# Performance work log

Hardware: AMD Instinct MI355X
Metric: run time of the kernel (lower is better)

The kernel has to match this reference:

```python
import jax, jax.numpy as jnp
import numpy as np

B, N, D, H, O = 4096, 128, 64, 256, 128  # batch, memory_size, memory_dim, controller_dim, output_size


def setup_inputs() -> dict:
    key = jax.random.key(0)
    ks = jax.random.split(key, 20)
    s = 0.05
    inp = {
        "x": jax.random.normal(ks[0], (B, O), jnp.float32),
        "memory": jax.random.normal(ks[1], (B, N, D), jnp.float32),
        "h": jax.random.normal(ks[2], (B, H), jnp.float32),
        "c": jax.random.normal(ks[3], (B, H), jnp.float32),
        # LSTMCell params (torch layout: gates ordered i, f, g, o; input = x||read_vec of width O+D)
        "W_ih": jax.random.normal(ks[4], (4 * H, O + D), jnp.float32) * s,
        "W_hh": jax.random.normal(ks[5], (4 * H, H), jnp.float32) * s,
        "b_ih": jax.random.normal(ks[6], (4 * H,), jnp.float32) * s,
        "b_hh": jax.random.normal(ks[7], (4 * H,), jnp.float32) * s,
        "W_read": jax.random.normal(ks[8], (N, H), jnp.float32) * s,
        "b_read": jax.random.normal(ks[9], (N,), jnp.float32) * s,
        "W_write": jax.random.normal(ks[10], (N, H), jnp.float32) * s,
        "b_write": jax.random.normal(ks[11], (N,), jnp.float32) * s,
        "W_erase": jax.random.normal(ks[12], (D, H), jnp.float32) * s,
        "b_erase": jax.random.normal(ks[13], (D,), jnp.float32) * s,
        "W_add": jax.random.normal(ks[14], (D, H), jnp.float32) * s,
        "b_add": jax.random.normal(ks[15], (D,), jnp.float32) * s,
        "W_out": jax.random.normal(ks[16], (O, H + D), jnp.float32) * s,
        "b_out": jax.random.normal(ks[17], (O,), jnp.float32) * s,
    }
    return inp


def reference(x, memory, h, c, W_ih, W_hh, b_ih, b_hh, W_read, b_read,
              W_write, b_write, W_erase, b_erase, W_add, b_add, W_out, b_out):
    # read: softmax attention over memory rows, addressed by previous hidden state
    read_w = jax.nn.softmax(h @ W_read.T + b_read, axis=-1)          # [B, N]
    read_vec = jnp.einsum("bn,bnd->bd", read_w, memory)               # [B, D]

    # LSTMCell step (torch gate order: i, f, g, o)
    ctrl_in = jnp.concatenate([x, read_vec], axis=-1)                 # [B, O+D]
    gates = ctrl_in @ W_ih.T + b_ih + h @ W_hh.T + b_hh               # [B, 4H]
    i, f, g, o = jnp.split(gates, 4, axis=-1)
    i, f, o = jax.nn.sigmoid(i), jax.nn.sigmoid(f), jax.nn.sigmoid(o)
    g = jnp.tanh(g)
    c_new = f * c + i * g
    h_new = o * jnp.tanh(c_new)

    # write: outer-product erase/add update
    write_w = jax.nn.softmax(h_new @ W_write.T + b_write, axis=-1)    # [B, N]
    erase = jax.nn.sigmoid(h_new @ W_erase.T + b_erase)               # [B, D]
    add = jnp.tanh(h_new @ W_add.T + b_add)                           # [B, D]
    ww = write_w[:, :, None]                                          # [B, N, 1]
    mem_new = memory * (1.0 - ww * erase[:, None, :]) + ww * add[:, None, :]

    out = jnp.concatenate([h_new, read_vec], axis=-1) @ W_out.T + b_out  # [B, O]
    return (out, mem_new, h_new, c_new)
```

## Files before the change

kernel.cpp:

```cpp
#include <hip/hip_runtime.h>
#include <math.h>


typedef __attribute__((ext_vector_type(8))) short bf16x8;
typedef __attribute__((ext_vector_type(4))) float f32x4;
typedef __attribute__((ext_vector_type(4))) unsigned short us4;

#define MFMA16(a, b, c) __builtin_amdgcn_mfma_f32_16x16x32_bf16(a, b, c, 0, 0, 0)
#define GLL16(gp, lp) __builtin_amdgcn_global_load_lds( \
    (const __attribute__((address_space(1))) void*)(gp), \
    (__attribute__((address_space(3))) void*)(lp), 16, 0, 0)
#define SW(row, s) ((s) ^ ((row) & 3))

__device__ __forceinline__ float sigf(float v) { return 1.f / (1.f + __expf(-v)); }

__device__ __forceinline__ unsigned short f2bf(float f) {
    unsigned u = __builtin_bit_cast(unsigned, f);
    u = (u + 0x7FFFu + ((u >> 16) & 1u)) >> 16;
    return (unsigned short)u;
}

__global__ __launch_bounds__(256) void kA_prep(
    const float* __restrict__ Wih, const float* __restrict__ Whh,
    const float* __restrict__ bih, const float* __restrict__ bhh,
    const float* __restrict__ Wr, const float* __restrict__ br,
    const float* __restrict__ Ww, const float* __restrict__ We,
    const float* __restrict__ Wa, const float* __restrict__ bw,
    const float* __restrict__ be, const float* __restrict__ ba,
    const float* __restrict__ Wo, const float* __restrict__ x,
    const float* __restrict__ h, const float* __restrict__ mem,
    unsigned short* __restrict__ Wg, float* __restrict__ bsum,
    unsigned short* __restrict__ Wh_b, float* __restrict__ bh_b,
    unsigned short* __restrict__ Wo_b, unsigned short* __restrict__ Ag,
    unsigned short* __restrict__ Aout)
{
    __shared__ unsigned short As[16 * 32];
    __shared__ unsigned short Bs[128 * 32];
    __shared__ float sc[16][128];
    __shared__ float wL[16][128];
    __shared__ float part[16][68];

    int t = threadIdx.x;
    int wid = t >> 6, lane = t & 63;
    int cl = lane & 15, ks = lane >> 4;
    int b0 = blockIdx.x * 16;

    int idx = blockIdx.x * 256 + t;
    int stride = gridDim.x * 256;
    for (int i = idx; i < 1024 * 448; i += stride) {
        int r = i / 448, cc = i - r * 448;
        float v = (cc < 192) ? Wih[(size_t)r * 192 + cc] : Whh[(size_t)r * 256 + (cc - 192)];
        Wg[i] = f2bf(v);
    }
    for (int i = idx; i < 1024; i += stride) bsum[i] = bih[i] + bhh[i];
    for (int i = idx; i < 256 * 256; i += stride) {
        int r = i >> 8, cc = i & 255;
        float v = (r < 128) ? Ww[(size_t)r * 256 + cc]
                : (r < 192) ? We[(size_t)(r - 128) * 256 + cc]
                            : Wa[(size_t)(r - 192) * 256 + cc];
        Wh_b[i] = f2bf(v);
    }
    for (int i = idx; i < 256; i += stride)
        bh_b[i] = (i < 128) ? bw[i] : (i < 192 ? be[i - 128] : ba[i - 192]);
    for (int i = idx; i < 128 * 320; i += stride) Wo_b[i] = f2bf(Wo[i]);
    for (int i = idx; i < 4096 * 96; i += stride) {
        int row = i / 96, j = i - row * 96;
        float4 v = (j < 32) ? ((const float4*)(x + (size_t)row * 128))[j]
                            : ((const float4*)(h + (size_t)row * 256))[j - 32];
        us4 o = { f2bf(v.x), f2bf(v.y), f2bf(v.z), f2bf(v.w) };
        int col = (j < 32) ? j * 4 : 192 + (j - 32) * 4;
        *(us4*)(Ag + (size_t)row * 448 + col) = o;
    }

    int aOff = cl * 32 + SW(cl, ks) * 8;
    int bOff[4];
#pragma unroll
    for (int f = 0; f < 4; ++f) {
        int br_ = (wid * 4 + f) * 16 + cl;
        bOff[f] = br_ * 32 + SW(br_, ks) * 8;
    }
    f32x4 acc[4] = {};
    for (int kc = 0; kc < 8; ++kc) {
        __syncthreads();
        {
            int row = t >> 4, k0 = (t & 15) * 2;
            float2 hv = *(const float2*)(h + (size_t)(b0 + row) * 256 + kc * 32 + k0);
            unsigned pk = (unsigned)f2bf(hv.x) | ((unsigned)f2bf(hv.y) << 16);
            *(unsigned*)(As + row * 32 + SW(row, k0 >> 3) * 8 + (k0 & 7)) = pk;
        }
        {
            int row = t >> 1, k0 = (t & 1) * 16;
            const float4* wp = (const float4*)(Wr + (size_t)row * 256 + kc * 32 + k0);
            float4 w0 = wp[0], w1 = wp[1], w2 = wp[2], w3 = wp[3];
            us4 p0 = { f2bf(w0.x), f2bf(w0.y), f2bf(w0.z), f2bf(w0.w) };
            us4 p1 = { f2bf(w1.x), f2bf(w1.y), f2bf(w1.z), f2bf(w1.w) };
            us4 p2 = { f2bf(w2.x), f2bf(w2.y), f2bf(w2.z), f2bf(w2.w) };
            us4 p3 = { f2bf(w3.x), f2bf(w3.y), f2bf(w3.z), f2bf(w3.w) };
            int g0 = k0 >> 3;
            unsigned short* basep = Bs + row * 32;
            *(us4*)(basep + SW(row, g0) * 8)     = p0;
            *(us4*)(basep + SW(row, g0) * 8 + 4) = p1;
            *(us4*)(basep + SW(row, g0 + 1) * 8)     = p2;
            *(us4*)(basep + SW(row, g0 + 1) * 8 + 4) = p3;
        }
        __syncthreads();
        if (wid < 2) {
            bf16x8 a = *(const bf16x8*)(As + aOff);
#pragma unroll
            for (int f = 0; f < 4; ++f)
                acc[f] = MFMA16(a, *(const bf16x8*)(Bs + bOff[f]), acc[f]);
        }
    }
    if (wid < 2) {
#pragma unroll
        for (int f = 0; f < 4; ++f)
#pragma unroll
            for (int r = 0; r < 4; ++r)
                sc[ks * 4 + r][(wid * 4 + f) * 16 + cl] = acc[f][r];
    }
    __syncthreads();
    {
        int row = t >> 4, l = t & 15;
        float v[8];
#pragma unroll
        for (int j = 0; j < 8; ++j) v[j] = sc[row][l + 16 * j] + br[l + 16 * j];
        float m = v[0];
#pragma unroll
        for (int j = 1; j < 8; ++j) m = fmaxf(m, v[j]);
#pragma unroll
        for (int mk = 8; mk >= 1; mk >>= 1) m = fmaxf(m, __shfl_xor(m, mk));
        float s = 0.f;
#pragma unroll
        for (int j = 0; j < 8; ++j) { v[j] = __expf(v[j] - m); s += v[j]; }
#pragma unroll
        for (int mk = 8; mk >= 1; mk >>= 1) s += __shfl_xor(s, mk);
        float inv = 1.f / s;
#pragma unroll
        for (int j = 0; j < 8; ++j) wL[row][l + 16 * j] = v[j] * inv;
    }
    __syncthreads();

    int np = t >> 4, d4 = t & 15;
    for (int r = 0; r < 16; ++r) {
        int row = b0 + r;
        const f32x4* m4 = (const f32x4*)(mem + (size_t)row * 8192);
        f32x4 a4 = { 0.f, 0.f, 0.f, 0.f };
#pragma unroll
        for (int j = 0; j < 8; ++j) {
            float w = wL[r][np + 16 * j];
            f32x4 mv = m4[t + 256 * j];
            a4 += w * mv;
        }
        part[np][d4 * 4 + 0] = a4[0]; part[np][d4 * 4 + 1] = a4[1];
        part[np][d4 * 4 + 2] = a4[2]; part[np][d4 * 4 + 3] = a4[3];
        __syncthreads();
        if (t < 64) {
            float s = 0.f;
#pragma unroll
            for (int q = 0; q < 16; ++q) s += part[q][t];
            unsigned short bv = f2bf(s);
            Ag[(size_t)row * 448 + 128 + t] = bv;
            Aout[(size_t)row * 320 + 256 + t] = bv;
        }
        __syncthreads();
    }
}

__global__ __launch_bounds__(256) void kB_gates(
    const unsigned short* __restrict__ Ag, const unsigned short* __restrict__ Wg,
    const float* __restrict__ bsum, const float* __restrict__ c,
    float* __restrict__ h_new, float* __restrict__ c_new,
    unsigned short* __restrict__ Aout)
{
    __shared__ unsigned short As[64 * 32];
    __shared__ unsigned short Bs[256 * 32];
    int t = threadIdx.x;
    int wid = t >> 6, lane = t & 63;
    int cl = lane & 15, ks = lane >> 4;
    int b0 = blockIdx.x * 64;
    int u0 = blockIdx.y * 64;

    int arow = t >> 2;
    const unsigned short* aSrc = Ag + (size_t)(b0 + arow) * 448 + SW(arow, t & 3) * 8;
    unsigned short* aDst = As + wid * 512;
    const unsigned short* bSrc[4];
    unsigned short* bDst[4];
#pragma unroll
    for (int j = 0; j < 4; ++j) {
        int rl = (j * 256 + t) >> 2;
        int g = rl >> 6, u = rl & 63;
        bSrc[j] = Wg + (size_t)(g * 256 + u0 + u) * 448 + SW(rl, t & 3) * 8;
        bDst[j] = Bs + (j * 256 + wid * 64) * 8;
    }

    int aOff[4];
#pragma unroll
    for (int rf = 0; rf < 4; ++rf) {
        int mr = rf * 16 + cl;
        aOff[rf] = mr * 32 + SW(mr, ks) * 8;
    }
    int bOff[4];
#pragma unroll
    for (int g = 0; g < 4; ++g) {
        int br_ = g * 64 + wid * 16 + cl;
        bOff[g] = br_ * 32 + SW(br_, ks) * 8;
    }

    f32x4 acc[4][4] = {};
    for (int kc = 0; kc < 14; ++kc) {
        __syncthreads();
        GLL16(aSrc, aDst);
        GLL16(bSrc[0], bDst[0]); GLL16(bSrc[1], bDst[1]);
        GLL16(bSrc[2], bDst[2]); GLL16(bSrc[3], bDst[3]);
        aSrc += 32;
#pragma unroll
        for (int j = 0; j < 4; ++j) bSrc[j] += 32;
        __syncthreads();
        bf16x8 a[4], b[4];
#pragma unroll
        for (int rf = 0; rf < 4; ++rf) a[rf] = *(const bf16x8*)(As + aOff[rf]);
#pragma unroll
        for (int g = 0; g < 4; ++g) b[g] = *(const bf16x8*)(Bs + bOff[g]);
#pragma unroll
        for (int rf = 0; rf < 4; ++rf)
#pragma unroll
            for (int g = 0; g < 4; ++g)
                acc[rf][g] = MFMA16(a[rf], b[g], acc[rf][g]);
    }

    int unit = u0 + wid * 16 + cl;
    float bi = bsum[unit], bf_ = bsum[256 + unit];
    float bg = bsum[512 + unit], bo_ = bsum[768 + unit];
#pragma unroll
    for (int rf = 0; rf < 4; ++rf) {
#pragma unroll
        for (int r = 0; r < 4; ++r) {
            int row = b0 + rf * 16 + ks * 4 + r;
            float iv = sigf(acc[rf][0][r] + bi);
            float fv = sigf(acc[rf][1][r] + bf_);
            float gv = tanhf(acc[rf][2][r] + bg);
            float ov = sigf(acc[rf][3][r] + bo_);
            float cv = fv * c[(size_t)row * 256 + unit] + iv * gv;
            float hv = ov * tanhf(cv);
            c_new[(size_t)row * 256 + unit] = cv;
            h_new[(size_t)row * 256 + unit] = hv;
            Aout[(size_t)row * 320 + unit] = f2bf(hv);
        }
    }
}

__global__ __launch_bounds__(256) void kC_heads_out_mem(
    const unsigned short* __restrict__ Aout, const unsigned short* __restrict__ Wh_b,
    const unsigned short* __restrict__ Wo_b, const float* __restrict__ bh_b,
    const float* __restrict__ bo, const float* __restrict__ mem,
    float* __restrict__ outp, float* __restrict__ mem_new)
{
    __shared__ unsigned short As[16 * 32];
    __shared__ unsigned short Bh[256 * 32];
    __shared__ unsigned short Bo[128 * 32];
    __shared__ float sc[16][256];
    __shared__ __align__(16) float wL[16][128];
    __shared__ __align__(16) float eL[16][64];
    __shared__ __align__(16) float aL[16][64];

    int t = threadIdx.x;
    int wid = t >> 6, lane = t & 63;
    int cl = lane & 15, ks = lane >> 4;
    int b0 = blockIdx.x * 16;

    const unsigned short* aSrc = Aout + (size_t)(b0 + (lane >> 2)) * 320 + SW(lane >> 2, lane & 3) * 8;
    const unsigned short* bhSrc[4];
    unsigned short* bhDst[4];
#pragma unroll
    for (int j = 0; j < 4; ++j) {
        int rl = (j * 256 + t) >> 2;
        bhSrc[j] = Wh_b + (size_t)rl * 256 + SW(rl, t & 3) * 8;
        bhDst[j] = Bh + (j * 256 + wid * 64) * 8;
    }
    const unsigned short* boSrc[2];
    unsigned short* boDst[2];
#pragma unroll
    for (int j = 0; j < 2; ++j) {
        int rj = j * 64 + (t >> 2);
        boSrc[j] = Wo_b + (size_t)rj * 320 + SW(rj, t & 3) * 8;
        boDst[j] = Bo + j * 2048 + wid * 512;
    }

    int aOff = cl * 32 + SW(cl, ks) * 8;
    int bOffH[4], bOffO[2];
#pragma unroll
    for (int f = 0; f < 4; ++f) { int br_ = (wid * 4 + f) * 16 + cl; bOffH[f] = br_ * 32 + SW(br_, ks) * 8; }
#pragma unroll
    for (int f = 0; f < 2; ++f) { int br_ = (wid * 2 + f) * 16 + cl; bOffO[f] = br_ * 32 + SW(br_, ks) * 8; }

    f32x4 accH[4] = {};
    f32x4 accO[2] = {};
    for (int kc = 0; kc < 10; ++kc) {
        __syncthreads();
        if (t < 64) GLL16(aSrc, As);
        if (kc < 8) {
            GLL16(bhSrc[0], bhDst[0]); GLL16(bhSrc[1], bhDst[1]);
            GLL16(bhSrc[2], bhDst[2]); GLL16(bhSrc[3], bhDst[3]);
        }
        GLL16(boSrc[0], boDst[0]); GLL16(boSrc[1], boDst[1]);
        aSrc += 32;
#pragma unroll
        for (int j = 0; j < 4; ++j) bhSrc[j] += 32;
#pragma unroll
        for (int j = 0; j < 2; ++j) boSrc[j] += 32;
        __syncthreads();
        bf16x8 a = *(const bf16x8*)(As + aOff);
        if (kc < 8) {
#pragma unroll
            for (int f = 0; f < 4; ++f)
                accH[f] = MFMA16(a, *(const bf16x8*)(Bh + bOffH[f]), accH[f]);
        }
#pragma unroll
        for (int f = 0; f < 2; ++f)
            accO[f] = MFMA16(a, *(const bf16x8*)(Bo + bOffO[f]), accO[f]);
    }

#pragma unroll
    for (int f = 0; f < 4; ++f) {
        int col = (wid * 4 + f) * 16 + cl;
        float bb = bh_b[col];
#pragma unroll
        for (int r = 0; r < 4; ++r)
            sc[ks * 4 + r][col] = accH[f][r] + bb;
    }
#pragma unroll
    for (int f = 0; f < 2; ++f) {
        int col = (wid * 2 + f) * 16 + cl;
        float bb = bo[col];
#pragma unroll
        for (int r = 0; r < 4; ++r)
            outp[(size_t)(b0 + ks * 4 + r) * 128 + col] = accO[f][r] + bb;
    }
    __syncthreads();
    {
        int row = t >> 4, l = t & 15;
        float v[8];
#pragma unroll
        for (int j = 0; j < 8; ++j) v[j] = sc[row][l + 16 * j];
        float m = v[0];
#pragma unroll
        for (int j = 1; j < 8; ++j) m = fmaxf(m, v[j]);
#pragma unroll
        for (int mk = 8; mk >= 1; mk >>= 1) m = fmaxf(m, __shfl_xor(m, mk));
        float s = 0.f;
#pragma unroll
        for (int j = 0; j < 8; ++j) { v[j] = __expf(v[j] - m); s += v[j]; }
#pragma unroll
        for (int mk = 8; mk >= 1; mk >>= 1) s += __shfl_xor(s, mk);
        float inv = 1.f / s;
#pragma unroll
        for (int j = 0; j < 8; ++j) wL[row][l + 16 * j] = v[j] * inv;
#pragma unroll
        for (int j = 0; j < 4; ++j) eL[row][l + 16 * j] = sigf(sc[row][128 + l + 16 * j]);
#pragma unroll
        for (int j = 0; j < 4; ++j) aL[row][l + 16 * j] = tanhf(sc[row][192 + l + 16 * j]);
    }
    __syncthreads();

    int np = t >> 4, d4 = t & 15;
    for (int r = 0; r < 16; ++r) {
        int row = b0 + r;
        const f32x4* m4 = (const f32x4*)(mem + (size_t)row * 8192);
        f32x4* o4 = (f32x4*)(mem_new + (size_t)row * 8192);
        f32x4 e4 = *(const f32x4*)&eL[r][d4 * 4];
        f32x4 a4 = *(const f32x4*)&aL[r][d4 * 4];
#pragma unroll
        for (int j = 0; j < 8; ++j) {
            float w = wL[r][np + 16 * j];
            f32x4 m = m4[t + 256 * j];
            f32x4 rr;
            rr[0] = m[0] * (1.f - w * e4[0]) + w * a4[0];
            rr[1] = m[1] * (1.f - w * e4[1]) + w * a4[1];
            rr[2] = m[2] * (1.f - w * e4[2]) + w * a4[2];
            rr[3] = m[3] * (1.f - w * e4[3]) + w * a4[3];
            __builtin_nontemporal_store(rr, &o4[t + 256 * j]);
        }
    }
}

extern "C" void kernel_launch(void* const* d_in, const int* in_sizes, int n_in,
                              void* d_out, int out_size, void* d_ws, size_t ws_size,
                              hipStream_t stream)
{
    const float* x    = (const float*)d_in[0];
    const float* mem  = (const float*)d_in[1];
    const float* h    = (const float*)d_in[2];
    const float* c    = (const float*)d_in[3];
    const float* Wih  = (const float*)d_in[4];
    const float* Whh  = (const float*)d_in[5];
    const float* bih  = (const float*)d_in[6];
    const float* bhh  = (const float*)d_in[7];
    const float* Wr   = (const float*)d_in[8];
    const float* br   = (const float*)d_in[9];
    const float* Ww   = (const float*)d_in[10];
    const float* bw   = (const float*)d_in[11];
    const float* We   = (const float*)d_in[12];
    const float* be   = (const float*)d_in[13];
    const float* Wa   = (const float*)d_in[14];
    const float* ba   = (const float*)d_in[15];
    const float* Wo   = (const float*)d_in[16];
    const float* bo   = (const float*)d_in[17];

    float* out     = (float*)d_out;
    float* mem_new = out + 524288;
    float* h_new   = out + 34078720;
    float* c_new   = out + 35127296;

    float* ws   = (float*)d_ws;
    float* bsum = ws;
    float* bh_b = ws + 1024;
    unsigned short* ub   = (unsigned short*)(ws + 1280);
    unsigned short* Ag   = ub;
    unsigned short* Aout = ub + 1835008;
    unsigned short* Wg   = ub + 3145728;
    unsigned short* Wh_b = ub + 3604480;
    unsigned short* Wo_b = ub + 3670016;

    kA_prep<<<256, 256, 0, stream>>>(Wih, Whh, bih, bhh, Wr, br, Ww, We, Wa, bw, be, ba,
                                     Wo, x, h, mem, Wg, bsum, Wh_b, bh_b, Wo_b, Ag, Aout);
    kB_gates<<<dim3(64, 4), 256, 0, stream>>>(Ag, Wg, bsum, c, h_new, c_new, Aout);
    kC_heads_out_mem<<<256, 256, 0, stream>>>(Aout, Wh_b, Wo_b, bh_b, bo, mem, out, mem_new);
}
```

Baseline: 106.6 us.

## Fuse read, LSTM gates, heads and memory update into one per-batch-tile kernel

Replaces the three-kernel pipeline (prep+read, gates GEMM, heads+memory update) with a weight-packing kernel and a single fused kernel processing 8 batch rows per block. Activations (x, h, read vector, h_new) stay in LDS as bf16 instead of round-tripping through global workspace buffers. MFMA B-operands are loaded directly from global memory without LDS staging. Gate weights are reordered so each block computes all four gates per unit chunk. The tradeoff is that every block rereads the full gate weight matrix from L2, with 16-row MFMA tiles only half used for 8 rows.

```diff
diff --git a/kernel.cpp b/kernel.cpp
--- a/kernel.cpp
+++ b/kernel.cpp
@@ -7,10 +7,6 @@
 typedef __attribute__((ext_vector_type(4))) unsigned short us4;
 
 #define MFMA16(a, b, c) __builtin_amdgcn_mfma_f32_16x16x32_bf16(a, b, c, 0, 0, 0)
-#define GLL16(gp, lp) __builtin_amdgcn_global_load_lds( \
-    (const __attribute__((address_space(1))) void*)(gp), \
-    (__attribute__((address_space(3))) void*)(lp), 16, 0, 0)
-#define SW(row, s) ((s) ^ ((row) & 3))
 
 __device__ __forceinline__ float sigf(float v) { return 1.f / (1.f + __expf(-v)); }
 
@@ -20,39 +16,31 @@
     return (unsigned short)u;
 }
 
-__global__ __launch_bounds__(256) void kA_prep(
+__device__ __forceinline__ int swaddr(int r, int c, int COLS) {
+    return r * COLS + (c & ~31) + ((((c >> 3) & 3) ^ (r & 3)) << 3) + (c & 7);
+}
+
+__global__ __launch_bounds__(256) void p_pack(
     const float* __restrict__ Wih, const float* __restrict__ Whh,
     const float* __restrict__ bih, const float* __restrict__ bhh,
-    const float* __restrict__ Wr, const float* __restrict__ br,
-    const float* __restrict__ Ww, const float* __restrict__ We,
-    const float* __restrict__ Wa, const float* __restrict__ bw,
-    const float* __restrict__ be, const float* __restrict__ ba,
-    const float* __restrict__ Wo, const float* __restrict__ x,
-    const float* __restrict__ h, const float* __restrict__ mem,
-    unsigned short* __restrict__ Wg, float* __restrict__ bsum,
-    unsigned short* __restrict__ Wh_b, float* __restrict__ bh_b,
-    unsigned short* __restrict__ Wo_b, unsigned short* __restrict__ Ag,
-    unsigned short* __restrict__ Aout)
+    const float* __restrict__ Wr, const float* __restrict__ Ww,
+    const float* __restrict__ We, const float* __restrict__ Wa,
+    const float* __restrict__ bw, const float* __restrict__ be,
+    const float* __restrict__ ba, const float* __restrict__ Wo,
+    unsigned short* __restrict__ Wg, unsigned short* __restrict__ Wr_b,
+    unsigned short* __restrict__ Wh_b, unsigned short* __restrict__ Wo_b,
+    float* __restrict__ bsum, float* __restrict__ bh_b)
 {
-    __shared__ unsigned short As[16 * 32];
-    __shared__ unsigned short Bs[128 * 32];
-    __shared__ float sc[16][128];
-    __shared__ float wL[16][128];
-    __shared__ float part[16][68];
-
-    int t = threadIdx.x;
-    int wid = t >> 6, lane = t & 63;
-    int cl = lane & 15, ks = lane >> 4;
-    int b0 = blockIdx.x * 16;
-
-    int idx = blockIdx.x * 256 + t;
+    int idx = blockIdx.x * 256 + threadIdx.x;
     int stride = gridDim.x * 256;
     for (int i = idx; i < 1024 * 448; i += stride) {
-        int r = i / 448, cc = i - r * 448;
-        float v = (cc < 192) ? Wih[(size_t)r * 192 + cc] : Whh[(size_t)r * 256 + (cc - 192)];
+        int p = i / 448, k = i - p * 448;
+        int uc = p >> 8, g = (p >> 6) & 3, ul = p & 63;
+        int R = g * 256 + uc * 64 + ul;
+        float v = (k < 192) ? Wih[(size_t)R * 192 + k] : Whh[(size_t)R * 256 + (k - 192)];
         Wg[i] = f2bf(v);
     }
-    for (int i = idx; i < 1024; i += stride) bsum[i] = bih[i] + bhh[i];
+    for (int i = idx; i < 128 * 256; i += stride) Wr_b[i] = f2bf(Wr[i]);
     for (int i = idx; i < 256 * 256; i += stride) {
         int r = i >> 8, cc = i & 255;
         float v = (r < 128) ? Ww[(size_t)r * 256 + cc]
@@ -60,66 +48,72 @@
                             : Wa[(size_t)(r - 192) * 256 + cc];
         Wh_b[i] = f2bf(v);
     }
+    for (int i = idx; i < 128 * 320; i += stride) Wo_b[i] = f2bf(Wo[i]);
+    for (int i = idx; i < 1024; i += stride) bsum[i] = bih[i] + bhh[i];
     for (int i = idx; i < 256; i += stride)
         bh_b[i] = (i < 128) ? bw[i] : (i < 192 ? be[i - 128] : ba[i - 192]);
-    for (int i = idx; i < 128 * 320; i += stride) Wo_b[i] = f2bf(Wo[i]);
-    for (int i = idx; i < 4096 * 96; i += stride) {
-        int row = i / 96, j = i - row * 96;
-        float4 v = (j < 32) ? ((const float4*)(x + (size_t)row * 128))[j]
-                            : ((const float4*)(h + (size_t)row * 256))[j - 32];
-        us4 o = { f2bf(v.x), f2bf(v.y), f2bf(v.z), f2bf(v.w) };
-        int col = (j < 32) ? j * 4 : 192 + (j - 32) * 4;
-        *(us4*)(Ag + (size_t)row * 448 + col) = o;
-    }
-
-    int aOff = cl * 32 + SW(cl, ks) * 8;
-    int bOff[4];
-#pragma unroll
-    for (int f = 0; f < 4; ++f) {
-        int br_ = (wid * 4 + f) * 16 + cl;
-        bOff[f] = br_ * 32 + SW(br_, ks) * 8;
-    }
-    f32x4 acc[4] = {};
-    for (int kc = 0; kc < 8; ++kc) {
-        __syncthreads();
-        {
-            int row = t >> 4, k0 = (t & 15) * 2;
-            float2 hv = *(const float2*)(h + (size_t)(b0 + row) * 256 + kc * 32 + k0);
-            unsigned pk = (unsigned)f2bf(hv.x) | ((unsigned)f2bf(hv.y) << 16);
-            *(unsigned*)(As + row * 32 + SW(row, k0 >> 3) * 8 + (k0 & 7)) = pk;
-        }
-        {
-            int row = t >> 1, k0 = (t & 1) * 16;
-            const float4* wp = (const float4*)(Wr + (size_t)row * 256 + kc * 32 + k0);
-            float4 w0 = wp[0], w1 = wp[1], w2 = wp[2], w3 = wp[3];
-            us4 p0 = { f2bf(w0.x), f2bf(w0.y), f2bf(w0.z), f2bf(w0.w) };
-            us4 p1 = { f2bf(w1.x), f2bf(w1.y), f2bf(w1.z), f2bf(w1.w) };
-            us4 p2 = { f2bf(w2.x), f2bf(w2.y), f2bf(w2.z), f2bf(w2.w) };
-            us4 p3 = { f2bf(w3.x), f2bf(w3.y), f2bf(w3.z), f2bf(w3.w) };
-            int g0 = k0 >> 3;
-            unsigned short* basep = Bs + row * 32;
-            *(us4*)(basep + SW(row, g0) * 8)     = p0;
-            *(us4*)(basep + SW(row, g0) * 8 + 4) = p1;
-            *(us4*)(basep + SW(row, g0 + 1) * 8)     = p2;
-            *(us4*)(basep + SW(row, g0 + 1) * 8 + 4) = p3;
-        }
-        __syncthreads();
-        if (wid < 2) {
-            bf16x8 a = *(const bf16x8*)(As + aOff);
-#pragma unroll
-            for (int f = 0; f < 4; ++f)
-                acc[f] = MFMA16(a, *(const bf16x8*)(Bs + bOff[f]), acc[f]);
-        }
-    }
-    if (wid < 2) {
-#pragma unroll
-        for (int f = 0; f < 4; ++f)
-#pragma unroll
-            for (int r = 0; r < 4; ++r)
-                sc[ks * 4 + r][(wid * 4 + f) * 16 + cl] = acc[f][r];
-    }
-    __syncthreads();
-    {
+}
+
+__global__ __launch_bounds__(256) void mega(
+    const float* __restrict__ x, const float* __restrict__ h,
+    const float* __restrict__ c, const float* __restrict__ mem,
+    const unsigned short* __restrict__ Wg, const unsigned short* __restrict__ Wr_b,
+    const unsigned short* __restrict__ Wh_b, const unsigned short* __restrict__ Wo_b,
+    const float* __restrict__ bsum, const float* __restrict__ bh_b,
+    const float* __restrict__ br, const float* __restrict__ bo,
+    float* __restrict__ outp, float* __restrict__ mem_new,
+    float* __restrict__ h_new, float* __restrict__ c_new)
+{
+    __shared__ unsigned short Agl[16 * 448];
+    __shared__ unsigned short hA[16 * 320];
+    __shared__ float sc[8][256];
+    __shared__ float wL[8][128];
+    __shared__ __align__(16) float eL[8][64];
+    __shared__ __align__(16) float aL[8][64];
+
+    int t = threadIdx.x;
+    int w = t >> 6, lane = t & 63;
+    int cl = lane & 15, ks = lane >> 4;
+    int b0 = blockIdx.x * 8;
+
+    {
+        int row = t >> 5, q = t & 31;
+        f32x4 v = *(const f32x4*)(x + (size_t)(b0 + row) * 128 + q * 4);
+        us4 o = { f2bf(v[0]), f2bf(v[1]), f2bf(v[2]), f2bf(v[3]) };
+        *(us4*)(Agl + swaddr(row, q * 4, 448)) = o;
+
+        const f32x4* hp = (const f32x4*)(h + (size_t)(b0 + row) * 256 + q * 8);
+        f32x4 v0 = hp[0], v1 = hp[1];
+        us4 o0 = { f2bf(v0[0]), f2bf(v0[1]), f2bf(v0[2]), f2bf(v0[3]) };
+        us4 o1 = { f2bf(v1[0]), f2bf(v1[1]), f2bf(v1[2]), f2bf(v1[3]) };
+        int a0 = swaddr(row, 192 + q * 8, 448);
+        *(us4*)(Agl + a0) = o0;
+        *(us4*)(Agl + a0 + 4) = o1;
+    }
+    __syncthreads();
+
+    {
+        f32x4 acc0 = {0.f, 0.f, 0.f, 0.f}, acc1 = {0.f, 0.f, 0.f, 0.f};
+        int col0 = (w * 2 + 0) * 16 + cl, col1 = (w * 2 + 1) * 16 + cl;
+        const unsigned short* bp0 = Wr_b + (size_t)col0 * 256 + ks * 8;
+        const unsigned short* bp1 = Wr_b + (size_t)col1 * 256 + ks * 8;
+#pragma unroll
+        for (int kc = 0; kc < 8; ++kc) {
+            bf16x8 a = *(const bf16x8*)(Agl + swaddr(cl, 192 + kc * 32 + ks * 8, 448));
+            acc0 = MFMA16(a, *(const bf16x8*)(bp0 + kc * 32), acc0);
+            acc1 = MFMA16(a, *(const bf16x8*)(bp1 + kc * 32), acc1);
+        }
+        if (ks < 2) {
+#pragma unroll
+            for (int r = 0; r < 4; ++r) {
+                sc[ks * 4 + r][col0] = acc0[r];
+                sc[ks * 4 + r][col1] = acc1[r];
+            }
+        }
+    }
+    __syncthreads();
+
+    if (t < 128) {
         int row = t >> 4, l = t & 15;
         float v[8];
 #pragma unroll
@@ -140,204 +134,120 @@
     }
     __syncthreads();
 
-    int np = t >> 4, d4 = t & 15;
-    for (int r = 0; r < 16; ++r) {
-        int row = b0 + r;
-        const f32x4* m4 = (const f32x4*)(mem + (size_t)row * 8192);
-        f32x4 a4 = { 0.f, 0.f, 0.f, 0.f };
-#pragma unroll
-        for (int j = 0; j < 8; ++j) {
-            float w = wL[r][np + 16 * j];
-            f32x4 mv = m4[t + 256 * j];
-            a4 += w * mv;
-        }
-        part[np][d4 * 4 + 0] = a4[0]; part[np][d4 * 4 + 1] = a4[1];
-        part[np][d4 * 4 + 2] = a4[2]; part[np][d4 * 4 + 3] = a4[3];
-        __syncthreads();
-        if (t < 64) {
-            float s = 0.f;
-#pragma unroll
-            for (int q = 0; q < 16; ++q) s += part[q][t];
-            unsigned short bv = f2bf(s);
-            Ag[(size_t)row * 448 + 128 + t] = bv;
-            Aout[(size_t)row * 320 + 256 + t] = bv;
-        }
-        __syncthreads();
-    }
-}
-
-__global__ __launch_bounds__(256) void kB_gates(
-    const unsigned short* __restrict__ Ag, const unsigned short* __restrict__ Wg,
-    const float* __restrict__ bsum, const float* __restrict__ c,
-    float* __restrict__ h_new, float* __restrict__ c_new,
-    unsigned short* __restrict__ Aout)
-{
-    __shared__ unsigned short As[64 * 32];
-    __shared__ unsigned short Bs[256 * 32];
-    int t = threadIdx.x;
-    int wid = t >> 6, lane = t & 63;
-    int cl = lane & 15, ks = lane >> 4;
-    int b0 = blockIdx.x * 64;
-    int u0 = blockIdx.y * 64;
-
-    int arow = t >> 2;
-    const unsigned short* aSrc = Ag + (size_t)(b0 + arow) * 448 + SW(arow, t & 3) * 8;
-    unsigned short* aDst = As + wid * 512;
-    const unsigned short* bSrc[4];
-    unsigned short* bDst[4];
-#pragma unroll
-    for (int j = 0; j < 4; ++j) {
-        int rl = (j * 256 + t) >> 2;
-        int g = rl >> 6, u = rl & 63;
-        bSrc[j] = Wg + (size_t)(g * 256 + u0 + u) * 448 + SW(rl, t & 3) * 8;
-        bDst[j] = Bs + (j * 256 + wid * 64) * 8;
-    }
-
-    int aOff[4];
-#pragma unroll
-    for (int rf = 0; rf < 4; ++rf) {
-        int mr = rf * 16 + cl;
-        aOff[rf] = mr * 32 + SW(mr, ks) * 8;
-    }
-    int bOff[4];
-#pragma unroll
-    for (int g = 0; g < 4; ++g) {
-        int br_ = g * 64 + wid * 16 + cl;
-        bOff[g] = br_ * 32 + SW(br_, ks) * 8;
-    }
-
-    f32x4 acc[4][4] = {};
-    for (int kc = 0; kc < 14; ++kc) {
-        __syncthreads();
-        GLL16(aSrc, aDst);
-        GLL16(bSrc[0], bDst[0]); GLL16(bSrc[1], bDst[1]);
-        GLL16(bSrc[2], bDst[2]); GLL16(bSrc[3], bDst[3]);
-        aSrc += 32;
-#pragma unroll
-        for (int j = 0; j < 4; ++j) bSrc[j] += 32;
-        __syncthreads();
-        bf16x8 a[4], b[4];
-#pragma unroll
-        for (int rf = 0; rf < 4; ++rf) a[rf] = *(const bf16x8*)(As + aOff[rf]);
-#pragma unroll
-        for (int g = 0; g < 4; ++g) b[g] = *(const bf16x8*)(Bs + bOff[g]);
-#pragma unroll
-        for (int rf = 0; rf < 4; ++rf)
-#pragma unroll
-            for (int g = 0; g < 4; ++g)
-                acc[rf][g] = MFMA16(a[rf], b[g], acc[rf][g]);
-    }
-
-    int unit = u0 + wid * 16 + cl;
-    float bi = bsum[unit], bf_ = bsum[256 + unit];
-    float bg = bsum[512 + unit], bo_ = bsum[768 + unit];
-#pragma unroll
-    for (int rf = 0; rf < 4; ++rf) {
-#pragma unroll
-        for (int r = 0; r < 4; ++r) {
-            int row = b0 + rf * 16 + ks * 4 + r;
-            float iv = sigf(acc[rf][0][r] + bi);
-            float fv = sigf(acc[rf][1][r] + bf_);
-            float gv = tanhf(acc[rf][2][r] + bg);
-            float ov = sigf(acc[rf][3][r] + bo_);
-            float cv = fv * c[(size_t)row * 256 + unit] + iv * gv;
-            float hv = ov * tanhf(cv);
-            c_new[(size_t)row * 256 + unit] = cv;
-            h_new[(size_t)row * 256 + unit] = hv;
-            Aout[(size_t)row * 320 + unit] = f2bf(hv);
-        }
-    }
-}
-
-__global__ __launch_bounds__(256) void kC_heads_out_mem(
-    const unsigned short* __restrict__ Aout, const unsigned short* __restrict__ Wh_b,
-    const unsigned short* __restrict__ Wo_b, const float* __restrict__ bh_b,
-    const float* __restrict__ bo, const float* __restrict__ mem,
-    float* __restrict__ outp, float* __restrict__ mem_new)
-{
-    __shared__ unsigned short As[16 * 32];
-    __shared__ unsigned short Bh[256 * 32];
-    __shared__ unsigned short Bo[128 * 32];
-    __shared__ float sc[16][256];
-    __shared__ __align__(16) float wL[16][128];
-    __shared__ __align__(16) float eL[16][64];
-    __shared__ __align__(16) float aL[16][64];
-
-    int t = threadIdx.x;
-    int wid = t >> 6, lane = t & 63;
-    int cl = lane & 15, ks = lane >> 4;
-    int b0 = blockIdx.x * 16;
-
-    const unsigned short* aSrc = Aout + (size_t)(b0 + (lane >> 2)) * 320 + SW(lane >> 2, lane & 3) * 8;
-    const unsigned short* bhSrc[4];
-    unsigned short* bhDst[4];
-#pragma unroll
-    for (int j = 0; j < 4; ++j) {
-        int rl = (j * 256 + t) >> 2;
-        bhSrc[j] = Wh_b + (size_t)rl * 256 + SW(rl, t & 3) * 8;
-        bhDst[j] = Bh + (j * 256 + wid * 64) * 8;
-    }
-    const unsigned short* boSrc[2];
-    unsigned short* boDst[2];
-#pragma unroll
-    for (int j = 0; j < 2; ++j) {
-        int rj = j * 64 + (t >> 2);
-        boSrc[j] = Wo_b + (size_t)rj * 320 + SW(rj, t & 3) * 8;
-        boDst[j] = Bo + j * 2048 + wid * 512;
-    }
-
-    int aOff = cl * 32 + SW(cl, ks) * 8;
-    int bOffH[4], bOffO[2];
-#pragma unroll
-    for (int f = 0; f < 4; ++f) { int br_ = (wid * 4 + f) * 16 + cl; bOffH[f] = br_ * 32 + SW(br_, ks) * 8; }
-#pragma unroll
-    for (int f = 0; f < 2; ++f) { int br_ = (wid * 2 + f) * 16 + cl; bOffO[f] = br_ * 32 + SW(br_, ks) * 8; }
-
-    f32x4 accH[4] = {};
-    f32x4 accO[2] = {};
-    for (int kc = 0; kc < 10; ++kc) {
-        __syncthreads();
-        if (t < 64) GLL16(aSrc, As);
-        if (kc < 8) {
-            GLL16(bhSrc[0], bhDst[0]); GLL16(bhSrc[1], bhDst[1]);
-            GLL16(bhSrc[2], bhDst[2]); GLL16(bhSrc[3], bhDst[3]);
-        }
-        GLL16(boSrc[0], boDst[0]); GLL16(boSrc[1], boDst[1]);
-        aSrc += 32;
-#pragma unroll
-        for (int j = 0; j < 4; ++j) bhSrc[j] += 32;
-#pragma unroll
-        for (int j = 0; j < 2; ++j) boSrc[j] += 32;
-        __syncthreads();
-        bf16x8 a = *(const bf16x8*)(As + aOff);
-        if (kc < 8) {
-#pragma unroll
-            for (int f = 0; f < 4; ++f)
-                accH[f] = MFMA16(a, *(const bf16x8*)(Bh + bOffH[f]), accH[f]);
-        }
-#pragma unroll
-        for (int f = 0; f < 2; ++f)
-            accO[f] = MFMA16(a, *(const bf16x8*)(Bo + bOffO[f]), accO[f]);
-    }
-
-#pragma unroll
-    for (int f = 0; f < 4; ++f) {
-        int col = (wid * 4 + f) * 16 + cl;
-        float bb = bh_b[col];
-#pragma unroll
-        for (int r = 0; r < 4; ++r)
-            sc[ks * 4 + r][col] = accH[f][r] + bb;
-    }
-#pragma unroll
-    for (int f = 0; f < 2; ++f) {
-        int col = (wid * 2 + f) * 16 + cl;
-        float bb = bo[col];
-#pragma unroll
-        for (int r = 0; r < 4; ++r)
-            outp[(size_t)(b0 + ks * 4 + r) * 128 + col] = accO[f][r] + bb;
-    }
-    __syncthreads();
-    {
+    {
+        int dg = cl, ng = ks;
+#pragma unroll
+        for (int rr = 0; rr < 2; ++rr) {
+            int r = w * 2 + rr;
+            const f32x4* m4 = (const f32x4*)(mem + (size_t)(b0 + r) * 8192);
+            f32x4 acc = {0.f, 0.f, 0.f, 0.f};
+#pragma unroll
+            for (int j = 0; j < 32; ++j) {
+                int n = ng + 4 * j;
+                acc += wL[r][n] * m4[n * 16 + dg];
+            }
+#pragma unroll
+            for (int i = 0; i < 4; ++i) {
+                acc[i] += __shfl_xor(acc[i], 16);
+                acc[i] += __shfl_xor(acc[i], 32);
+            }
+            if (lane < 16) {
+                int d0 = dg * 4;
+                us4 o = { f2bf(acc[0]), f2bf(acc[1]), f2bf(acc[2]), f2bf(acc[3]) };
+                *(us4*)(Agl + swaddr(r, 128 + d0, 448)) = o;
+                *(us4*)(hA + swaddr(r, 256 + d0, 320)) = o;
+            }
+        }
+    }
+    __syncthreads();
+
+    {
+        bf16x8 aF[14];
+#pragma unroll
+        for (int kc = 0; kc < 14; ++kc)
+            aF[kc] = *(const bf16x8*)(Agl + swaddr(cl, kc * 32 + ks * 8, 448));
+#pragma unroll 1
+        for (int uc = 0; uc < 4; ++uc) {
+            f32x4 acc0 = {0.f,0.f,0.f,0.f}, acc1 = {0.f,0.f,0.f,0.f};
+            f32x4 acc2 = {0.f,0.f,0.f,0.f}, acc3 = {0.f,0.f,0.f,0.f};
+            const unsigned short* bp0 = Wg + (size_t)(uc * 256 +   0 + w * 16 + cl) * 448 + ks * 8;
+            const unsigned short* bp1 = Wg + (size_t)(uc * 256 +  64 + w * 16 + cl) * 448 + ks * 8;
+            const unsigned short* bp2 = Wg + (size_t)(uc * 256 + 128 + w * 16 + cl) * 448 + ks * 8;
+            const unsigned short* bp3 = Wg + (size_t)(uc * 256 + 192 + w * 16 + cl) * 448 + ks * 8;
+#pragma unroll
+            for (int kc = 0; kc < 14; ++kc) {
+                acc0 = MFMA16(aF[kc], *(const bf16x8*)(bp0 + kc * 32), acc0);
+                acc1 = MFMA16(aF[kc], *(const bf16x8*)(bp1 + kc * 32), acc1);
+                acc2 = MFMA16(aF[kc], *(const bf16x8*)(bp2 + kc * 32), acc2);
+                acc3 = MFMA16(aF[kc], *(const bf16x8*)(bp3 + kc * 32), acc3);
+            }
+            int unit = uc * 64 + w * 16 + cl;
+            float bi = bsum[unit], bf_ = bsum[256 + unit];
+            float bg = bsum[512 + unit], bo_ = bsum[768 + unit];
+            if (ks < 2) {
+#pragma unroll
+                for (int r = 0; r < 4; ++r) {
+                    int lrow = ks * 4 + r, row = b0 + lrow;
+                    float iv = sigf(acc0[r] + bi);
+                    float fv = sigf(acc1[r] + bf_);
+                    float gv = tanhf(acc2[r] + bg);
+                    float ov = sigf(acc3[r] + bo_);
+                    float cv = fv * c[(size_t)row * 256 + unit] + iv * gv;
+                    float hv = ov * tanhf(cv);
+                    c_new[(size_t)row * 256 + unit] = cv;
+                    h_new[(size_t)row * 256 + unit] = hv;
+                    hA[swaddr(lrow, unit, 320)] = f2bf(hv);
+                }
+            }
+        }
+    }
+    __syncthreads();
+
+    {
+        f32x4 accH0 = {0.f,0.f,0.f,0.f}, accH1 = {0.f,0.f,0.f,0.f};
+        f32x4 accH2 = {0.f,0.f,0.f,0.f}, accH3 = {0.f,0.f,0.f,0.f};
+        f32x4 accO0 = {0.f,0.f,0.f,0.f}, accO1 = {0.f,0.f,0.f,0.f};
+        const unsigned short* bh0 = Wh_b + (size_t)((w * 4 + 0) * 16 + cl) * 256 + ks * 8;
+        const unsigned short* bh1 = Wh_b + (size_t)((w * 4 + 1) * 16 + cl) * 256 + ks * 8;
+        const unsigned short* bh2 = Wh_b + (size_t)((w * 4 + 2) * 16 + cl) * 256 + ks * 8;
+        const unsigned short* bh3 = Wh_b + (size_t)((w * 4 + 3) * 16 + cl) * 256 + ks * 8;
+        const unsigned short* bo0 = Wo_b + (size_t)((w * 2 + 0) * 16 + cl) * 320 + ks * 8;
+        const unsigned short* bo1 = Wo_b + (size_t)((w * 2 + 1) * 16 + cl) * 320 + ks * 8;
+#pragma unroll
+        for (int kc = 0; kc < 10; ++kc) {
+            bf16x8 a = *(const bf16x8*)(hA + swaddr(cl, kc * 32 + ks * 8, 320));
+            if (kc < 8) {
+                accH0 = MFMA16(a, *(const bf16x8*)(bh0 + kc * 32), accH0);
+                accH1 = MFMA16(a, *(const bf16x8*)(bh1 + kc * 32), accH1);
+                accH2 = MFMA16(a, *(const bf16x8*)(bh2 + kc * 32), accH2);
+                accH3 = MFMA16(a, *(const bf16x8*)(bh3 + kc * 32), accH3);
+            }
+            accO0 = MFMA16(a, *(const bf16x8*)(bo0 + kc * 32), accO0);
+            accO1 = MFMA16(a, *(const bf16x8*)(bo1 + kc * 32), accO1);
+        }
+        if (ks < 2) {
+            f32x4 aH[4] = { accH0, accH1, accH2, accH3 };
+#pragma unroll
+            for (int f = 0; f < 4; ++f) {
+                int col = (w * 4 + f) * 16 + cl;
+                float bb = bh_b[col];
+#pragma unroll
+                for (int r = 0; r < 4; ++r) sc[ks * 4 + r][col] = aH[f][r] + bb;
+            }
+            f32x4 aO[2] = { accO0, accO1 };
+#pragma unroll
+            for (int f = 0; f < 2; ++f) {
+                int col = (w * 2 + f) * 16 + cl;
+                float bb = bo[col];
+#pragma unroll
+                for (int r = 0; r < 4; ++r)
+                    outp[(size_t)(b0 + ks * 4 + r) * 128 + col] = aO[f][r] + bb;
+            }
+        }
+    }
+    __syncthreads();
+
+    if (t < 128) {
         int row = t >> 4, l = t & 15;
         float v[8];
 #pragma unroll
@@ -362,23 +272,24 @@
     }
     __syncthreads();
 
-    int np = t >> 4, d4 = t & 15;
-    for (int r = 0; r < 16; ++r) {
-        int row = b0 + r;
-        const f32x4* m4 = (const f32x4*)(mem + (size_t)row * 8192);
-        f32x4* o4 = (f32x4*)(mem_new + (size_t)row * 8192);
-        f32x4 e4 = *(const f32x4*)&eL[r][d4 * 4];
-        f32x4 a4 = *(const f32x4*)&aL[r][d4 * 4];
-#pragma unroll
-        for (int j = 0; j < 8; ++j) {
-            float w = wL[r][np + 16 * j];
-            f32x4 m = m4[t + 256 * j];
-            f32x4 rr;
-            rr[0] = m[0] * (1.f - w * e4[0]) + w * a4[0];
-            rr[1] = m[1] * (1.f - w * e4[1]) + w * a4[1];
-            rr[2] = m[2] * (1.f - w * e4[2]) + w * a4[2];
-            rr[3] = m[3] * (1.f - w * e4[3]) + w * a4[3];
-            __builtin_nontemporal_store(rr, &o4[t + 256 * j]);
+    {
+        int dg = cl, ng = ks;
+        f32x4 one = {1.f, 1.f, 1.f, 1.f};
+#pragma unroll
+        for (int rr = 0; rr < 2; ++rr) {
+            int r = w * 2 + rr;
+            const f32x4* m4 = (const f32x4*)(mem + (size_t)(b0 + r) * 8192);
+            f32x4* o4 = (f32x4*)(mem_new + (size_t)(b0 + r) * 8192);
+            f32x4 e4 = *(const f32x4*)&eL[r][dg * 4];
+            f32x4 a4 = *(const f32x4*)&aL[r][dg * 4];
+#pragma unroll
+            for (int j = 0; j < 32; ++j) {
+                int n = ng + 4 * j;
+                float wv = wL[r][n];
+                f32x4 m = m4[n * 16 + dg];
+                f32x4 res = m * (one - e4 * wv) + a4 * wv;
+                __builtin_nontemporal_store(res, &o4[n * 16 + dg]);
+            }
         }
     }
 }
@@ -415,14 +326,13 @@
     float* bsum = ws;
     float* bh_b = ws + 1024;
     unsigned short* ub   = (unsigned short*)(ws + 1280);
-    unsigned short* Ag   = ub;
-    unsigned short* Aout = ub + 1835008;
-    unsigned short* Wg   = ub + 3145728;
-    unsigned short* Wh_b = ub + 3604480;
-    unsigned short* Wo_b = ub + 3670016;
-
-    kA_prep<<<256, 256, 0, stream>>>(Wih, Whh, bih, bhh, Wr, br, Ww, We, Wa, bw, be, ba,
-                                     Wo, x, h, mem, Wg, bsum, Wh_b, bh_b, Wo_b, Ag, Aout);
-    kB_gates<<<dim3(64, 4), 256, 0, stream>>>(Ag, Wg, bsum, c, h_new, c_new, Aout);
-    kC_heads_out_mem<<<256, 256, 0, stream>>>(Aout, Wh_b, Wo_b, bh_b, bo, mem, out, mem_new);
-}
+    unsigned short* Wg   = ub;
+    unsigned short* Wr_b = ub + 458752;
+    unsigned short* Wh_b = ub + 491520;
+    unsigned short* Wo_b = ub + 557056;
+
+    p_pack<<<256, 256, 0, stream>>>(Wih, Whh, bih, bhh, Wr, Ww, We, Wa, bw, be, ba, Wo,
+                                    Wg, Wr_b, Wh_b, Wo_b, bsum, bh_b);
+    mega<<<512, 256, 0, stream>>>(x, h, c, mem, Wg, Wr_b, Wh_b, Wo_b, bsum, bh_b, br, bo,
+                                  out, mem_new, h_new, c_new);
+}
```

Result: slower. 196.1 us (+83.9%).

## Split memory read and write passes into separate per-row kernels

Applied to the files above, without the earlier changes.

The memory-bound read-vector reduction and the erase/add memory update move out of the 256-block GEMM kernels into dedicated kernels launched with one block per batch row (4096 blocks). The GEMM kernels now write the softmax weights, erase and add vectors to workspace instead of keeping them in shared memory. The goal is more parallelism and better HBM saturation for the 128 MB memory streams, which previously ran serially inside 256 blocks with syncthreads per row. In exchange there are two more kernel launches and extra workspace traffic for the intermediate weights.

```diff
diff --git a/kernel.cpp b/kernel.cpp
--- a/kernel.cpp
+++ b/kernel.cpp
@@ -28,17 +28,15 @@
     const float* __restrict__ Wa, const float* __restrict__ bw,
     const float* __restrict__ be, const float* __restrict__ ba,
     const float* __restrict__ Wo, const float* __restrict__ x,
-    const float* __restrict__ h, const float* __restrict__ mem,
+    const float* __restrict__ h,
     unsigned short* __restrict__ Wg, float* __restrict__ bsum,
     unsigned short* __restrict__ Wh_b, float* __restrict__ bh_b,
     unsigned short* __restrict__ Wo_b, unsigned short* __restrict__ Ag,
-    unsigned short* __restrict__ Aout)
+    float* __restrict__ read_w)
 {
     __shared__ unsigned short As[16 * 32];
     __shared__ unsigned short Bs[128 * 32];
     __shared__ float sc[16][128];
-    __shared__ float wL[16][128];
-    __shared__ float part[16][68];
 
     int t = threadIdx.x;
     int wid = t >> 6, lane = t & 63;
@@ -136,33 +134,38 @@
         for (int mk = 8; mk >= 1; mk >>= 1) s += __shfl_xor(s, mk);
         float inv = 1.f / s;
 #pragma unroll
-        for (int j = 0; j < 8; ++j) wL[row][l + 16 * j] = v[j] * inv;
-    }
+        for (int j = 0; j < 8; ++j)
+            read_w[(size_t)(b0 + row) * 128 + l + 16 * j] = v[j] * inv;
+    }
+}
+
+__global__ __launch_bounds__(256) void k2_read_vec(
+    const float* __restrict__ mem, const float* __restrict__ read_w,
+    unsigned short* __restrict__ Ag, unsigned short* __restrict__ Aout)
+{
+    __shared__ float part[16][68];
+    int t = threadIdx.x;
+    int b = blockIdx.x;
+    int np = t >> 4, d4 = t & 15;
+    const float4* m4 = (const float4*)(mem + (size_t)b * 8192);
+    float4 acc = make_float4(0.f, 0.f, 0.f, 0.f);
+#pragma unroll
+    for (int j = 0; j < 8; ++j) {
+        int n = np + 16 * j;
+        float w = read_w[(size_t)b * 128 + n];
+        float4 mv = m4[t + 256 * j];
+        acc.x += w * mv.x; acc.y += w * mv.y; acc.z += w * mv.z; acc.w += w * mv.w;
+    }
+    part[np][d4 * 4 + 0] = acc.x; part[np][d4 * 4 + 1] = acc.y;
+    part[np][d4 * 4 + 2] = acc.z; part[np][d4 * 4 + 3] = acc.w;
     __syncthreads();
-
-    int np = t >> 4, d4 = t & 15;
-    for (int r = 0; r < 16; ++r) {
-        int row = b0 + r;
-        const f32x4* m4 = (const f32x4*)(mem + (size_t)row * 8192);
-        f32x4 a4 = { 0.f, 0.f, 0.f, 0.f };
-#pragma unroll
-        for (int j = 0; j < 8; ++j) {
-            float w = wL[r][np + 16 * j];
-            f32x4 mv = m4[t + 256 * j];
-            a4 += w * mv;
-        }
-        part[np][d4 * 4 + 0] = a4[0]; part[np][d4 * 4 + 1] = a4[1];
-        part[np][d4 * 4 + 2] = a4[2]; part[np][d4 * 4 + 3] = a4[3];
-        __syncthreads();
-        if (t < 64) {
-            float s = 0.f;
-#pragma unroll
-            for (int q = 0; q < 16; ++q) s += part[q][t];
-            unsigned short bv = f2bf(s);
-            Ag[(size_t)row * 448 + 128 + t] = bv;
-            Aout[(size_t)row * 320 + 256 + t] = bv;
-        }
-        __syncthreads();
+    if (t < 64) {
+        float s = 0.f;
+#pragma unroll
+        for (int q = 0; q < 16; ++q) s += part[q][t];
+        unsigned short bv = f2bf(s);
+        Ag[(size_t)b * 448 + 128 + t] = bv;
+        Aout[(size_t)b * 320 + 256 + t] = bv;
     }
 }
 
@@ -249,19 +252,16 @@
     }
 }
 
-__global__ __launch_bounds__(256) void kC_heads_out_mem(
+__global__ __launch_bounds__(256) void kC_heads_out(
     const unsigned short* __restrict__ Aout, const unsigned short* __restrict__ Wh_b,
     const unsigned short* __restrict__ Wo_b, const float* __restrict__ bh_b,
-    const float* __restrict__ bo, const float* __restrict__ mem,
-    float* __restrict__ outp, float* __restrict__ mem_new)
+    const float* __restrict__ bo, float* __restrict__ write_w,
+    float* __restrict__ erase, float* __restrict__ addv, float* __restrict__ outp)
 {
     __shared__ unsigned short As[16 * 32];
     __shared__ unsigned short Bh[256 * 32];
     __shared__ unsigned short Bo[128 * 32];
     __shared__ float sc[16][256];
-    __shared__ __align__(16) float wL[16][128];
-    __shared__ __align__(16) float eL[16][64];
-    __shared__ __align__(16) float aL[16][64];
 
     int t = threadIdx.x;
     int wid = t >> 6, lane = t & 63;
@@ -353,33 +353,41 @@
 #pragma unroll
         for (int mk = 8; mk >= 1; mk >>= 1) s += __shfl_xor(s, mk);
         float inv = 1.f / s;
-#pragma unroll
-        for (int j = 0; j < 8; ++j) wL[row][l + 16 * j] = v[j] * inv;
-#pragma unroll
-        for (int j = 0; j < 4; ++j) eL[row][l + 16 * j] = sigf(sc[row][128 + l + 16 * j]);
-#pragma unroll
-        for (int j = 0; j < 4; ++j) aL[row][l + 16 * j] = tanhf(sc[row][192 + l + 16 * j]);
-    }
-    __syncthreads();
-
-    int np = t >> 4, d4 = t & 15;
-    for (int r = 0; r < 16; ++r) {
-        int row = b0 + r;
-        const f32x4* m4 = (const f32x4*)(mem + (size_t)row * 8192);
-        f32x4* o4 = (f32x4*)(mem_new + (size_t)row * 8192);
-        f32x4 e4 = *(const f32x4*)&eL[r][d4 * 4];
-        f32x4 a4 = *(const f32x4*)&aL[r][d4 * 4];
-#pragma unroll
-        for (int j = 0; j < 8; ++j) {
-            float w = wL[r][np + 16 * j];
-            f32x4 m = m4[t + 256 * j];
-            f32x4 rr;
-            rr[0] = m[0] * (1.f - w * e4[0]) + w * a4[0];
-            rr[1] = m[1] * (1.f - w * e4[1]) + w * a4[1];
-            rr[2] = m[2] * (1.f - w * e4[2]) + w * a4[2];
-            rr[3] = m[3] * (1.f - w * e4[3]) + w * a4[3];
-            __builtin_nontemporal_store(rr, &o4[t + 256 * j]);
-        }
+        int row_g = b0 + row;
+#pragma unroll
+        for (int j = 0; j < 8; ++j)
+            write_w[(size_t)row_g * 128 + l + 16 * j] = v[j] * inv;
+#pragma unroll
+        for (int j = 0; j < 4; ++j)
+            erase[(size_t)row_g * 64 + l + 16 * j] = sigf(sc[row][128 + l + 16 * j]);
+#pragma unroll
+        for (int j = 0; j < 4; ++j)
+            addv[(size_t)row_g * 64 + l + 16 * j] = tanhf(sc[row][192 + l + 16 * j]);
+    }
+}
+
+__global__ __launch_bounds__(256) void k5_mem_update(
+    const float* __restrict__ mem, const float* __restrict__ write_w,
+    const float* __restrict__ erase, const float* __restrict__ addv,
+    float* __restrict__ mem_new)
+{
+    int t = threadIdx.x; int b = blockIdx.x;
+    int np = t >> 4, d0 = (t & 15) * 4;
+    const f32x4* m4 = (const f32x4*)(mem + (size_t)b * 8192);
+    f32x4* o4 = (f32x4*)(mem_new + (size_t)b * 8192);
+    f32x4 e4 = *(const f32x4*)(erase + (size_t)b * 64 + d0);
+    f32x4 a4 = *(const f32x4*)(addv + (size_t)b * 64 + d0);
+#pragma unroll
+    for (int j = 0; j < 8; ++j) {
+        int n = np + 16 * j;
+        float w = write_w[(size_t)b * 128 + n];
+        f32x4 m = m4[t + 256 * j];
+        f32x4 r;
+        r[0] = m[0] * (1.f - w * e4[0]) + w * a4[0];
+        r[1] = m[1] * (1.f - w * e4[1]) + w * a4[1];
+        r[2] = m[2] * (1.f - w * e4[2]) + w * a4[2];
+        r[3] = m[3] * (1.f - w * e4[3]) + w * a4[3];
+        __builtin_nontemporal_store(r, &o4[t + 256 * j]);
     }
 }
 
@@ -411,10 +419,14 @@
     float* h_new   = out + 34078720;
     float* c_new   = out + 35127296;
 
-    float* ws   = (float*)d_ws;
-    float* bsum = ws;
-    float* bh_b = ws + 1024;
-    unsigned short* ub   = (unsigned short*)(ws + 1280);
+    float* ws      = (float*)d_ws;
+    float* read_w  = ws;
+    float* write_w = ws + 524288;
+    float* erase   = ws + 1048576;
+    float* addv    = ws + 1310720;
+    float* bsum    = ws + 1572864;
+    float* bh_b    = ws + 1573888;
+    unsigned short* ub   = (unsigned short*)(ws + 1574144);
     unsigned short* Ag   = ub;
     unsigned short* Aout = ub + 1835008;
     unsigned short* Wg   = ub + 3145728;
@@ -422,7 +434,10 @@
     unsigned short* Wo_b = ub + 3670016;
 
     kA_prep<<<256, 256, 0, stream>>>(Wih, Whh, bih, bhh, Wr, br, Ww, We, Wa, bw, be, ba,
-                                     Wo, x, h, mem, Wg, bsum, Wh_b, bh_b, Wo_b, Ag, Aout);
+                                     Wo, x, h, Wg, bsum, Wh_b, bh_b, Wo_b, Ag, read_w);
+    k2_read_vec<<<4096, 256, 0, stream>>>(mem, read_w, Ag, Aout);
     kB_gates<<<dim3(64, 4), 256, 0, stream>>>(Ag, Wg, bsum, c, h_new, c_new, Aout);
-    kC_heads_out_mem<<<256, 256, 0, stream>>>(Aout, Wh_b, Wo_b, bh_b, bo, mem, out, mem_new);
-}
+    kC_heads_out<<<256, 256, 0, stream>>>(Aout, Wh_b, Wo_b, bh_b, bo,
+                                          write_w, erase, addv, out);
+    k5_mem_update<<<4096, 256, 0, stream>>>(mem, write_w, erase, addv, mem_new);
+}
```

New measurement: 111.8 us. 4.9% more time.
